# Performance work log

Measured on AMD Instinct MI355X. Metric: run time of the kernel, lower is better.

## Reference

```python
import jax, jax.numpy as jnp
import numpy as np

B, N, C_IN, L, C_OUT = 8, 50000, 32, 9, 64
M, NNZ = 12500, 37500


def setup_inputs() -> dict:
    key = jax.random.key(0)
    k = jax.random.split(key, 7)
    x = jax.random.normal(k[0], (B, N, C_IN), dtype=jnp.float32)
    weight = jax.random.normal(k[1], (L * C_IN, C_OUT), dtype=jnp.float32) * (1.0 / np.sqrt(L * C_IN))
    bias = jax.random.normal(k[2], (C_OUT,), dtype=jnp.float32) * 0.01
    values = jax.random.uniform(k[3], (NNZ,), dtype=jnp.float32)
    spiral_indices = jax.random.randint(k[4], (N, L), 0, N, dtype=jnp.int64)
    rows = jax.random.randint(k[5], (NNZ,), 0, M, dtype=jnp.int64)
    cols = jax.random.randint(k[6], (NNZ,), 0, N, dtype=jnp.int64)
    return {"x": x, "weight": weight, "bias": bias, "values": values,
            "spiral_indices": spiral_indices, "rows": rows, "cols": cols,
            "num_out_verts": M}


def reference(x, weight, bias, values, spiral_indices, rows, cols, num_out_verts):
    b, n, c = x.shape
    # SpiralConv: gather spiral neighborhoods, flatten, linear
    g = x[:, spiral_indices]                      # [B, N, L, C]
    g = g.reshape(b, n, -1)                       # [B, N, L*C]
    out = jnp.einsum('bnk,ko->bno', g, weight) + bias
    out = jax.nn.elu(out)                         # [B, N, C_OUT]
    # Pool: sparse down_transform (gather, scale, scatter_add)
    gathered = out[:, cols] * values[None, :, None]          # [B, NNZ, C_OUT]
    pooled = jnp.zeros((b, num_out_verts, out.shape[-1]), dtype=out.dtype)
    pooled = pooled.at[:, rows].add(gathered)                # [B, M, C_OUT]
    return pooled
```

## Files before the change

### kernel.cpp

```cpp
#include <hip/hip_runtime.h>

#define BATCH   8
#define NVERT   50000
#define CIN     32
#define LSP     9
#define COUT    64
#define MVERT   12500
#define NNZ     37500

#define TILE_T  256
#define TPB     147
#define NFRAG   2304
#define OUTDW   (BATCH * MVERT * COUT)
#define XELEMS  (BATCH * NVERT * CIN)

#define PRE_BLOCKS  6250
#define PACK_BLOCKS 9
#define ZERO_BLOCKS 6250
#define HZ_BLOCKS   49

typedef __attribute__((ext_vector_type(8))) short  short8;
typedef __attribute__((ext_vector_type(4))) float  floatx4;

static __device__ __forceinline__ unsigned short f2bf(float f) {
    union { float f; unsigned int u; } c; c.f = f;
    unsigned int u = c.u;
    return (unsigned short)((u + 0x7fffu + ((u >> 16) & 1u)) >> 16);
}

__global__ __launch_bounds__(256)
void prep_kernel(const float* __restrict__ x, const float* __restrict__ w,
                 unsigned short* __restrict__ x16, unsigned short* __restrict__ wp,
                 float* __restrict__ out, int* __restrict__ hist)
{
    const int blk = blockIdx.x;
    const int tid = threadIdx.x;
    if (blk < PRE_BLOCKS) {
        const size_t base = ((size_t)blk * 256 + tid) * 8;
        const float4* s = (const float4*)(x + base);
        float4 a = s[0], c = s[1];
        unsigned short t[8];
        t[0]=f2bf(a.x); t[1]=f2bf(a.y); t[2]=f2bf(a.z); t[3]=f2bf(a.w);
        t[4]=f2bf(c.x); t[5]=f2bf(c.y); t[6]=f2bf(c.z); t[7]=f2bf(c.w);
        *(uint4*)(x16 + base) = *(uint4*)t;
    } else if (blk < PRE_BLOCKS + PACK_BLOCKS) {
        const int f = (blk - PRE_BLOCKS) * 256 + tid;
        if (f < NFRAG) {
            int s = f >> 8, g = (f >> 6) & 3, lane = f & 63;
            int k0 = s * 32 + (lane >> 4) * 8, col = g * 16 + (lane & 15);
            unsigned short t[8];
            #pragma unroll
            for (int j = 0; j < 8; ++j)
                t[j] = f2bf(w[(size_t)(k0 + j) * COUT + col]);
            ((uint4*)wp)[f] = *(uint4*)t;
        }
    } else if (blk < PRE_BLOCKS + PACK_BLOCKS + ZERO_BLOCKS) {
        const size_t base = ((size_t)(blk - PRE_BLOCKS - PACK_BLOCKS) * 256 + tid) * 4;
        if (base < OUTDW) *(uint4*)(out + base) = (uint4){0, 0, 0, 0};
    } else {
        const int i = (blk - PRE_BLOCKS - PACK_BLOCKS - ZERO_BLOCKS) * 256 + tid;
        if (i < MVERT) hist[i] = 0;
    }
}

__global__ __launch_bounds__(256)
void hist_kernel(const int* __restrict__ rows, int* __restrict__ hist) {
    int z = blockIdx.x * 256 + threadIdx.x;
    if (z < NNZ) atomicAdd(&hist[rows[z]], 1);
}

__global__ __launch_bounds__(1024)
void scan_kernel(const int* __restrict__ hist, int* __restrict__ off2) {
    __shared__ int sh[1024];
    const int t = threadIdx.x;
    const int base = t * 13;
    int loc[13];
    int s = 0;
    #pragma unroll
    for (int j = 0; j < 13; ++j) {
        int i = base + j;
        int v = (i < MVERT) ? hist[i] : 0;
        loc[j] = s; s += v;
    }
    sh[t] = s;
    __syncthreads();
    for (int d = 1; d < 1024; d <<= 1) {
        int v = (t >= d) ? sh[t - d] : 0;
        __syncthreads();
        sh[t] += v;
        __syncthreads();
    }
    const int excl = sh[t] - s;
    #pragma unroll
    for (int j = 0; j < 13; ++j) {
        int i = base + j;
        if (i < MVERT) off2[i] = excl + loc[j];
    }
}

__global__ __launch_bounds__(256)
void scatter_kernel(const int* __restrict__ rows, const int* __restrict__ cols,
                    const float* __restrict__ vals, int* __restrict__ off2,
                    int* __restrict__ rows_s, int* __restrict__ cols_s,
                    float* __restrict__ vals_s) {
    int z = blockIdx.x * 256 + threadIdx.x;
    if (z < NNZ) {
        int r = rows[z];
        int pos = atomicAdd(&off2[r], 1);
        rows_s[pos] = r;
        cols_s[pos] = cols[z];
        vals_s[pos] = vals[z];
    }
}

__global__ __launch_bounds__(256)
void spiral_mfma4_kernel(const unsigned short* __restrict__ x16,
                         const unsigned short* __restrict__ wp,
                         const float* __restrict__ bias,
                         const int* __restrict__ spiral,
                         const int* __restrict__ rows_s,
                         const int* __restrict__ cols_s,
                         const float* __restrict__ vals_s,
                         float* __restrict__ out)
{
    __shared__ float sS[4 * 16 * 68];

    const int bid  = blockIdx.x;
    const int b    = bid & 7;
    const int tile = bid >> 3;
    const int tid  = threadIdx.x;
    const int w    = tid >> 6;
    const int lane = tid & 63;
    const int quad = lane >> 4;
    const int m16  = lane & 15;
    const int z0w  = tile * TILE_T + 64 * w;

    const int   zc   = min(z0w + lane, NNZ - 1);
    const int   colv = cols_s[zc];
    const int   rowv = rows_s[zc];
    const float valv = vals_s[zc];

    int idx[9];
    #pragma unroll
    for (int s = 0; s < 9; ++s) idx[s] = spiral[colv * LSP + s];

    const unsigned short* xb = x16 + (size_t)b * NVERT * CIN;

    floatx4 acc[4][4];
    #pragma unroll
    for (int mt = 0; mt < 4; ++mt)
        #pragma unroll
        for (int g = 0; g < 4; ++g) acc[mt][g] = (floatx4){0.f, 0.f, 0.f, 0.f};

    #pragma unroll
    for (int s = 0; s < 9; ++s) {
        short8 bf[4];
        #pragma unroll
        for (int g = 0; g < 4; ++g)
            bf[g] = *(const short8*)(wp + (size_t)((s * 4 + g) * 64 + lane) * 8);
        #pragma unroll
        for (int mt = 0; mt < 4; ++mt) {
            int tix = __shfl(idx[s], mt * 16 + m16);
            short8 af = *(const short8*)(xb + (size_t)tix * CIN + quad * 8);
            #pragma unroll
            for (int g = 0; g < 4; ++g)
                acc[mt][g] = __builtin_amdgcn_mfma_f32_16x16x32_bf16(af, bf[g], acc[mt][g], 0, 0, 0);
        }
    }

    float* region = sS + w * (16 * 68);
    float bs[4];
    #pragma unroll
    for (int g = 0; g < 4; ++g) bs[g] = bias[g * 16 + m16];

    float* outb = out + (size_t)b * MVERT * COUT;

    #pragma unroll
    for (int mt = 0; mt < 4; ++mt) {
        const int zbase = z0w + mt * 16;
        int nval = NNZ - zbase;
        nval = (nval < 0) ? 0 : ((nval > 16) ? 16 : nval);
        if (nval <= 0) continue;

        #pragma unroll
        for (int r = 0; r < 4; ++r) {
            const int tt = quad * 4 + r;
            const float vv = __shfl(valv, mt * 16 + tt);
            #pragma unroll
            for (int g = 0; g < 4; ++g) {
                float y = acc[mt][g][r] + bs[g];
                y = (y > 0.0f) ? y : (__expf(y) - 1.0f);
                region[tt * 68 + g * 16 + m16] = y * vv;
            }
        }

        float a = 0.0f;
        int cur = __shfl(rowv, mt * 16);
        for (int t = 0; t < nval; ++t) {
            int rt = __shfl(rowv, mt * 16 + t);
            if (rt != cur) {
                atomicAdd(outb + (size_t)cur * COUT + lane, a);
                a = 0.0f; cur = rt;
            }
            a += region[t * 68 + lane];
        }
        atomicAdd(outb + (size_t)cur * COUT + lane, a);
    }
}

extern "C" void kernel_launch(void* const* d_in, const int* in_sizes, int n_in,
                              void* d_out, int out_size, void* d_ws, size_t ws_size,
                              hipStream_t stream) {
    const float* x      = (const float*)d_in[0];
    const float* w      = (const float*)d_in[1];
    const float* bias   = (const float*)d_in[2];
    const float* vals   = (const float*)d_in[3];
    const int*   spiral = (const int*)d_in[4];
    const int*   rows   = (const int*)d_in[5];
    const int*   cols   = (const int*)d_in[6];
    float* out = (float*)d_out;

    char* base = (char*)d_ws;
    unsigned short* wp     = (unsigned short*)(base);
    unsigned short* x16    = (unsigned short*)(base + 36864);
    int*            hist   = (int*)(base + 25636864);
    int*            off2   = (int*)(base + 25686864);
    int*            rows_s = (int*)(base + 25736864);
    int*            cols_s = (int*)(base + 25886880);
    float*          vals_s = (float*)(base + 26036896);

    const int prep_grid = PRE_BLOCKS + PACK_BLOCKS + ZERO_BLOCKS + HZ_BLOCKS;
    prep_kernel<<<prep_grid, 256, 0, stream>>>(x, w, x16, wp, out, hist);
    hist_kernel<<<147, 256, 0, stream>>>(rows, hist);
    scan_kernel<<<1, 1024, 0, stream>>>(hist, off2);
    scatter_kernel<<<147, 256, 0, stream>>>(rows, cols, vals, off2,
                                            rows_s, cols_s, vals_s);
    spiral_mfma4_kernel<<<BATCH * TPB, 256, 0, stream>>>(x16, wp, bias, spiral,
                                                         rows_s, cols_s, vals_s, out);
}
```

Before: 179.5 us.

## Precompute spiral indices, stage weights in LDS, double-buffer x gathers

Adds a kernel that resolves each sorted nonzero's spiral neighbour indices once into packed 16-bit form, so the 8 batch blocks no longer each repeat the dependent cols→spiral lookup. The main kernel loads the packed bf16 weight fragments into LDS via global_load_lds, and software-pipelines the x gathers by prefetching the next spiral step's rows while the MFMAs for the current step run. The cost is an extra kernel launch, more LDS per block (about 54KB), which limits occupancy, and a reliance on vertex indices fitting in 16 bits.

```diff
diff --git a/kernel.cpp b/kernel.cpp
--- a/kernel.cpp
+++ b/kernel.cpp
@@ -12,7 +12,6 @@
 #define TPB     147
 #define NFRAG   2304
 #define OUTDW   (BATCH * MVERT * COUT)
-#define XELEMS  (BATCH * NVERT * CIN)
 
 #define PRE_BLOCKS  6250
 #define PACK_BLOCKS 9
@@ -26,6 +25,15 @@
     union { float f; unsigned int u; } c; c.f = f;
     unsigned int u = c.u;
     return (unsigned short)((u + 0x7fffu + ((u >> 16) & 1u)) >> 16);
+}
+
+static __device__ __forceinline__ void dma16(const void* g, void* l) {
+    typedef __attribute__((address_space(1))) const void gvoid;
+    typedef __attribute__((address_space(3))) void lvoid;
+    __builtin_amdgcn_global_load_lds(
+        (gvoid*)(unsigned long long)g,
+        (lvoid*)(unsigned int)(unsigned long long)l,
+        16, 0, 0);
 }
 
 __global__ __launch_bounds__(256)
@@ -114,15 +122,32 @@
 }
 
 __global__ __launch_bounds__(256)
-void spiral_mfma4_kernel(const unsigned short* __restrict__ x16,
+void tidx_kernel(const int* __restrict__ cols_s, const int* __restrict__ spiral,
+                 unsigned short* __restrict__ tidx) {
+    int z = blockIdx.x * 256 + threadIdx.x;
+    if (z < NNZ) {
+        const int c = cols_s[z];
+        unsigned short t[16];
+        #pragma unroll
+        for (int s = 0; s < 9; ++s) t[s] = (unsigned short)spiral[c * LSP + s];
+        #pragma unroll
+        for (int s = 9; s < 16; ++s) t[s] = 0;
+        uint4* dst = (uint4*)(tidx + (size_t)z * 16);
+        dst[0] = *(uint4*)t;
+        dst[1] = *(uint4*)(t + 8);
+    }
+}
+
+__global__ __launch_bounds__(256, 3)
+void spiral_mfma5_kernel(const unsigned short* __restrict__ x16,
                          const unsigned short* __restrict__ wp,
                          const float* __restrict__ bias,
-                         const int* __restrict__ spiral,
+                         const unsigned short* __restrict__ tidx,
                          const int* __restrict__ rows_s,
-                         const int* __restrict__ cols_s,
                          const float* __restrict__ vals_s,
                          float* __restrict__ out)
 {
+    __shared__ uint4 sWP4[NFRAG];
     __shared__ float sS[4 * 16 * 68];
 
     const int bid  = blockIdx.x;
@@ -135,14 +160,21 @@
     const int m16  = lane & 15;
     const int z0w  = tile * TILE_T + 64 * w;
 
+    #pragma unroll
+    for (int i = 0; i < 9; ++i)
+        dma16(wp + (size_t)(i * 256 + tid) * 8, (char*)sWP4 + (i * 256 + tid) * 16);
+
     const int   zc   = min(z0w + lane, NNZ - 1);
-    const int   colv = cols_s[zc];
     const int   rowv = rows_s[zc];
     const float valv = vals_s[zc];
-
+    const uint4 p0 = *(const uint4*)(tidx + (size_t)zc * 16);
+    const uint  p1 = *(const unsigned int*)(tidx + (size_t)zc * 16 + 8);
     int idx[9];
-    #pragma unroll
-    for (int s = 0; s < 9; ++s) idx[s] = spiral[colv * LSP + s];
+    idx[0] = p0.x & 0xffff;  idx[1] = p0.x >> 16;
+    idx[2] = p0.y & 0xffff;  idx[3] = p0.y >> 16;
+    idx[4] = p0.z & 0xffff;  idx[5] = p0.z >> 16;
+    idx[6] = p0.w & 0xffff;  idx[7] = p0.w >> 16;
+    idx[8] = p1 & 0xffff;
 
     const unsigned short* xb = x16 + (size_t)b * NVERT * CIN;
 
@@ -152,19 +184,37 @@
         #pragma unroll
         for (int g = 0; g < 4; ++g) acc[mt][g] = (floatx4){0.f, 0.f, 0.f, 0.f};
 
+    __syncthreads();
+
+    const unsigned short* sWP = (const unsigned short*)sWP4;
+
+    short8 a_cur[4], a_nxt[4];
+    #pragma unroll
+    for (int mt = 0; mt < 4; ++mt) {
+        int tix = __shfl(idx[0], mt * 16 + m16);
+        a_cur[mt] = *(const short8*)(xb + (size_t)tix * CIN + quad * 8);
+    }
     #pragma unroll
     for (int s = 0; s < 9; ++s) {
+        if (s < 8) {
+            #pragma unroll
+            for (int mt = 0; mt < 4; ++mt) {
+                int tix = __shfl(idx[s + 1], mt * 16 + m16);
+                a_nxt[mt] = *(const short8*)(xb + (size_t)tix * CIN + quad * 8);
+            }
+        }
         short8 bf[4];
         #pragma unroll
         for (int g = 0; g < 4; ++g)
-            bf[g] = *(const short8*)(wp + (size_t)((s * 4 + g) * 64 + lane) * 8);
-        #pragma unroll
-        for (int mt = 0; mt < 4; ++mt) {
-            int tix = __shfl(idx[s], mt * 16 + m16);
-            short8 af = *(const short8*)(xb + (size_t)tix * CIN + quad * 8);
+            bf[g] = *(const short8*)(sWP + (size_t)((s * 4 + g) * 64 + lane) * 8);
+        #pragma unroll
+        for (int mt = 0; mt < 4; ++mt)
             #pragma unroll
             for (int g = 0; g < 4; ++g)
-                acc[mt][g] = __builtin_amdgcn_mfma_f32_16x16x32_bf16(af, bf[g], acc[mt][g], 0, 0, 0);
+                acc[mt][g] = __builtin_amdgcn_mfma_f32_16x16x32_bf16(a_cur[mt], bf[g], acc[mt][g], 0, 0, 0);
+        if (s < 8) {
+            #pragma unroll
+            for (int mt = 0; mt < 4; ++mt) a_cur[mt] = a_nxt[mt];
         }
     }
 
@@ -228,6 +278,7 @@
     int*            rows_s = (int*)(base + 25736864);
     int*            cols_s = (int*)(base + 25886880);
     float*          vals_s = (float*)(base + 26036896);
+    unsigned short* tidx   = (unsigned short*)(base + 26186912);
 
     const int prep_grid = PRE_BLOCKS + PACK_BLOCKS + ZERO_BLOCKS + HZ_BLOCKS;
     prep_kernel<<<prep_grid, 256, 0, stream>>>(x, w, x16, wp, out, hist);
@@ -235,6 +286,7 @@
     scan_kernel<<<1, 1024, 0, stream>>>(hist, off2);
     scatter_kernel<<<147, 256, 0, stream>>>(rows, cols, vals, off2,
                                             rows_s, cols_s, vals_s);
-    spiral_mfma4_kernel<<<BATCH * TPB, 256, 0, stream>>>(x16, wp, bias, spiral,
-                                                         rows_s, cols_s, vals_s, out);
-}
+    tidx_kernel<<<147, 256, 0, stream>>>(cols_s, spiral, tidx);
+    spiral_mfma5_kernel<<<BATCH * TPB, 256, 0, stream>>>(x16, wp, bias, tidx,
+                                                         rows_s, vals_s, out);
+}
```

After: 180.4 us. Within noise of the previous version (+0.5%).

## Precompute packed spiral indices per nnz, halve tile, prefetch gathers, drop LDS reduction

Applied to the files above, without the earlier changes.

The scatter pass now resolves each sorted nonzero's spiral neighbourhood and stores it as packed 16-bit indices, so the main kernel skips the dependent cols→spiral lookup. The main kernel uses 128-nnz tiles (32 per wave), loads all 18 A fragments up front before the MFMA loop, and replaces the LDS-staged segmented row reduction with an in-register segmented sum over each lane's 4 rows before the atomics. This aims to raise memory-level parallelism and occupancy and to cut LDS traffic, at the cost of more atomics and more registers. Storing indices as 16-bit assumes vertex ids fit below 65536, which holds for N=50000.

```diff
diff --git a/kernel.cpp b/kernel.cpp
--- a/kernel.cpp
+++ b/kernel.cpp
@@ -8,11 +8,11 @@
 #define MVERT   12500
 #define NNZ     37500
 
-#define TILE_T  256
-#define TPB     147
 #define NFRAG   2304
 #define OUTDW   (BATCH * MVERT * COUT)
-#define XELEMS  (BATCH * NVERT * CIN)
+
+#define TILE_T  128
+#define TPB     293
 
 #define PRE_BLOCKS  6250
 #define PACK_BLOCKS 9
@@ -100,31 +100,37 @@
 
 __global__ __launch_bounds__(256)
 void scatter_kernel(const int* __restrict__ rows, const int* __restrict__ cols,
-                    const float* __restrict__ vals, int* __restrict__ off2,
-                    int* __restrict__ rows_s, int* __restrict__ cols_s,
-                    float* __restrict__ vals_s) {
+                    const float* __restrict__ vals, const int* __restrict__ spiral,
+                    int* __restrict__ off2,
+                    int* __restrict__ rows_s, float* __restrict__ vals_s,
+                    unsigned short* __restrict__ tidx) {
     int z = blockIdx.x * 256 + threadIdx.x;
     if (z < NNZ) {
         int r = rows[z];
+        int c = cols[z];
         int pos = atomicAdd(&off2[r], 1);
         rows_s[pos] = r;
-        cols_s[pos] = cols[z];
         vals_s[pos] = vals[z];
-    }
-}
-
-__global__ __launch_bounds__(256)
-void spiral_mfma4_kernel(const unsigned short* __restrict__ x16,
+        unsigned short t[16];
+        #pragma unroll
+        for (int s = 0; s < 9; ++s) t[s] = (unsigned short)spiral[c * LSP + s];
+        #pragma unroll
+        for (int s = 9; s < 16; ++s) t[s] = 0;
+        uint4* dst = (uint4*)(tidx + (size_t)pos * 16);
+        dst[0] = *(uint4*)t;
+        dst[1] = *(uint4*)(t + 8);
+    }
+}
+
+__global__ __launch_bounds__(256, 3)
+void spiral_mfma6_kernel(const unsigned short* __restrict__ x16,
                          const unsigned short* __restrict__ wp,
                          const float* __restrict__ bias,
-                         const int* __restrict__ spiral,
+                         const unsigned short* __restrict__ tidx,
                          const int* __restrict__ rows_s,
-                         const int* __restrict__ cols_s,
                          const float* __restrict__ vals_s,
                          float* __restrict__ out)
 {
-    __shared__ float sS[4 * 16 * 68];
-
     const int bid  = blockIdx.x;
     const int b    = bid & 7;
     const int tile = bid >> 3;
@@ -133,22 +139,35 @@
     const int lane = tid & 63;
     const int quad = lane >> 4;
     const int m16  = lane & 15;
-    const int z0w  = tile * TILE_T + 64 * w;
-
-    const int   zc   = min(z0w + lane, NNZ - 1);
-    const int   colv = cols_s[zc];
+    const int z0w  = tile * TILE_T + 32 * w;
+
+    const int   zc   = min(z0w + (lane & 31), NNZ - 1);
     const int   rowv = rows_s[zc];
     const float valv = vals_s[zc];
-
+    const uint4 p0 = *(const uint4*)(tidx + (size_t)zc * 16);
+    const unsigned int p1 = *(const unsigned int*)(tidx + (size_t)zc * 16 + 8);
     int idx[9];
-    #pragma unroll
-    for (int s = 0; s < 9; ++s) idx[s] = spiral[colv * LSP + s];
+    idx[0] = p0.x & 0xffff;  idx[1] = p0.x >> 16;
+    idx[2] = p0.y & 0xffff;  idx[3] = p0.y >> 16;
+    idx[4] = p0.z & 0xffff;  idx[5] = p0.z >> 16;
+    idx[6] = p0.w & 0xffff;  idx[7] = p0.w >> 16;
+    idx[8] = p1 & 0xffff;
 
     const unsigned short* xb = x16 + (size_t)b * NVERT * CIN;
 
-    floatx4 acc[4][4];
-    #pragma unroll
-    for (int mt = 0; mt < 4; ++mt)
+    short8 A[2][9];
+    #pragma unroll
+    for (int s = 0; s < 9; ++s) {
+        #pragma unroll
+        for (int mt = 0; mt < 2; ++mt) {
+            int tix = __shfl(idx[s], mt * 16 + m16);
+            A[mt][s] = *(const short8*)(xb + (size_t)tix * CIN + quad * 8);
+        }
+    }
+
+    floatx4 acc[2][4];
+    #pragma unroll
+    for (int mt = 0; mt < 2; ++mt)
         #pragma unroll
         for (int g = 0; g < 4; ++g) acc[mt][g] = (floatx4){0.f, 0.f, 0.f, 0.f};
 
@@ -159,52 +178,48 @@
         for (int g = 0; g < 4; ++g)
             bf[g] = *(const short8*)(wp + (size_t)((s * 4 + g) * 64 + lane) * 8);
         #pragma unroll
-        for (int mt = 0; mt < 4; ++mt) {
-            int tix = __shfl(idx[s], mt * 16 + m16);
-            short8 af = *(const short8*)(xb + (size_t)tix * CIN + quad * 8);
+        for (int mt = 0; mt < 2; ++mt)
             #pragma unroll
             for (int g = 0; g < 4; ++g)
-                acc[mt][g] = __builtin_amdgcn_mfma_f32_16x16x32_bf16(af, bf[g], acc[mt][g], 0, 0, 0);
-        }
-    }
-
-    float* region = sS + w * (16 * 68);
+                acc[mt][g] = __builtin_amdgcn_mfma_f32_16x16x32_bf16(A[mt][s], bf[g], acc[mt][g], 0, 0, 0);
+    }
+
     float bs[4];
     #pragma unroll
     for (int g = 0; g < 4; ++g) bs[g] = bias[g * 16 + m16];
-
     float* outb = out + (size_t)b * MVERT * COUT;
 
     #pragma unroll
-    for (int mt = 0; mt < 4; ++mt) {
-        const int zbase = z0w + mt * 16;
-        int nval = NNZ - zbase;
-        nval = (nval < 0) ? 0 : ((nval > 16) ? 16 : nval);
-        if (nval <= 0) continue;
-
+    for (int mt = 0; mt < 2; ++mt) {
+        int   rr[4]; float vv[4]; bool val[4];
         #pragma unroll
         for (int r = 0; r < 4; ++r) {
-            const int tt = quad * 4 + r;
-            const float vv = __shfl(valv, mt * 16 + tt);
+            const int tsk = mt * 16 + quad * 4 + r;
+            rr[r]  = __shfl(rowv, tsk);
+            vv[r]  = __shfl(valv, tsk);
+            val[r] = (z0w + tsk) < NNZ;
+        }
+        bool emit[4];
+        #pragma unroll
+        for (int r = 0; r < 4; ++r)
+            emit[r] = (r == 3) || (!val[r + 1 > 3 ? 3 : r + 1]) || (rr[r + 1 > 3 ? 3 : r + 1] != rr[r]);
+        #pragma unroll
+        for (int g = 0; g < 4; ++g) {
+            const int ch = g * 16 + m16;
+            float s = 0.0f;
             #pragma unroll
-            for (int g = 0; g < 4; ++g) {
-                float y = acc[mt][g][r] + bs[g];
-                y = (y > 0.0f) ? y : (__expf(y) - 1.0f);
-                region[tt * 68 + g * 16 + m16] = y * vv;
+            for (int r = 0; r < 4; ++r) {
+                if (val[r]) {
+                    float y = acc[mt][g][r] + bs[g];
+                    y = (y > 0.0f) ? y : (__expf(y) - 1.0f);
+                    s += y * vv[r];
+                    if (emit[r]) {
+                        atomicAdd(outb + (size_t)rr[r] * COUT + ch, s);
+                        s = 0.0f;
+                    }
+                }
             }
         }
-
-        float a = 0.0f;
-        int cur = __shfl(rowv, mt * 16);
-        for (int t = 0; t < nval; ++t) {
-            int rt = __shfl(rowv, mt * 16 + t);
-            if (rt != cur) {
-                atomicAdd(outb + (size_t)cur * COUT + lane, a);
-                a = 0.0f; cur = rt;
-            }
-            a += region[t * 68 + lane];
-        }
-        atomicAdd(outb + (size_t)cur * COUT + lane, a);
     }
 }
 
@@ -226,15 +241,15 @@
     int*            hist   = (int*)(base + 25636864);
     int*            off2   = (int*)(base + 25686864);
     int*            rows_s = (int*)(base + 25736864);
-    int*            cols_s = (int*)(base + 25886880);
     float*          vals_s = (float*)(base + 26036896);
+    unsigned short* tidx   = (unsigned short*)(base + 26186912);
 
     const int prep_grid = PRE_BLOCKS + PACK_BLOCKS + ZERO_BLOCKS + HZ_BLOCKS;
     prep_kernel<<<prep_grid, 256, 0, stream>>>(x, w, x16, wp, out, hist);
     hist_kernel<<<147, 256, 0, stream>>>(rows, hist);
     scan_kernel<<<1, 1024, 0, stream>>>(hist, off2);
-    scatter_kernel<<<147, 256, 0, stream>>>(rows, cols, vals, off2,
-                                            rows_s, cols_s, vals_s);
-    spiral_mfma4_kernel<<<BATCH * TPB, 256, 0, stream>>>(x16, wp, bias, spiral,
-                                                         rows_s, cols_s, vals_s, out);
-}
+    scatter_kernel<<<147, 256, 0, stream>>>(rows, cols, vals, spiral, off2,
+                                            rows_s, vals_s, tidx);
+    spiral_mfma6_kernel<<<BATCH * TPB, 256, 0, stream>>>(x16, wp, bias, tidx,
+                                                         rows_s, vals_s, out);
+}
```

New measurement: 177.2 us. About the same (-1.2%).
